# Performance work log

Hardware: AMD Instinct MI355X
Metric: run time of the kernel (lower is better)

Reference implementation:

```python
import jax, jax.numpy as jnp
import numpy as np

DIM = 1024
NUM_HEADS = 16
HEAD_DIM = DIM // NUM_HEADS  # 64
SCALE = float(np.sqrt(HEAD_DIM))


def setup_inputs() -> dict:
    key = jax.random.key(0)
    k1, k2, k3, k4 = jax.random.split(key, 4)
    B, N = 2, 2048
    x = jax.random.normal(k1, (B, N, DIM), dtype=jnp.float32)
    # torch nn.Linear weights are [out_features, in_features]
    w_qkv = jax.random.normal(k2, (3 * DIM, DIM), dtype=jnp.float32) * (1.0 / np.sqrt(DIM))
    w_proj = jax.random.normal(k3, (DIM, DIM), dtype=jnp.float32) * (1.0 / np.sqrt(DIM))
    b_proj = jax.random.normal(k4, (DIM,), dtype=jnp.float32) * 0.02
    return {"x": x, "w_qkv": w_qkv, "w_proj": w_proj, "b_proj": b_proj}


def reference(x, w_qkv, w_proj, b_proj):
    B, N, C = x.shape
    H, D = NUM_HEADS, HEAD_DIM
    # qkv linear (no bias): [B,N,3C]
    qkv = jnp.einsum('bnc,oc->bno', x, w_qkv)
    qkv = qkv.reshape(B, N, 3, H, D).transpose(2, 0, 3, 1, 4)  # [3,B,H,N,D]
    q, k, v = qkv[0], qkv[1], qkv[2]
    attn = jnp.einsum('bhnd,bhmd->bhnm', q, k) / SCALE  # [B,H,N,N]
    attn = jax.nn.softmax(attn, axis=-1)
    out = jnp.einsum('bhnm,bhmd->bhnd', attn, v)  # [B,H,N,D]
    out = out.transpose(0, 2, 1, 3).reshape(B, N, C)
    return jnp.einsum('bnc,oc->bno', out, w_proj) + b_proj
```

## Files before the change

### kernel.cpp

```cpp
#include <hip/hip_runtime.h>


typedef __bf16 bf16x8 __attribute__((ext_vector_type(8)));
typedef __bf16 bf16x4 __attribute__((ext_vector_type(4)));
typedef float f32x4 __attribute__((ext_vector_type(4)));

#define NTOK 2048
#define MFMA16(a, b, c) __builtin_amdgcn_mfma_f32_16x16x32_bf16((a), (b), (c), 0, 0, 0)

#define WAITBAR(N)                                         \
    asm volatile("s_waitcnt vmcnt(" #N ")" ::: "memory"); \
    __builtin_amdgcn_s_barrier();                          \
    __builtin_amdgcn_sched_barrier(0)

__device__ __forceinline__ unsigned short f2bf(float f) {
    unsigned int u = __float_as_uint(f);
    u = (u + 0x7FFFu + ((u >> 16) & 1u)) >> 16;
    return (unsigned short)u;
}

__device__ __forceinline__ float hw_exp2(float x) {
#if __has_builtin(__builtin_amdgcn_exp2f)
    return __builtin_amdgcn_exp2f(x);
#else
    float r;
    asm("v_exp_f32 %0, %1" : "=v"(r) : "v"(x));
    return r;
#endif
}

__device__ __forceinline__ void gload16(const void* g, void* l) {
    __builtin_amdgcn_global_load_lds(
        (__attribute__((address_space(1))) void*)(g),
        (__attribute__((address_space(3))) void*)(l), 16, 0, 0);
}

__global__ __launch_bounds__(256) void cast3_kernel(
    const float* __restrict__ x, const float* __restrict__ wq,
    const float* __restrict__ wp, unsigned short* __restrict__ xb,
    unsigned short* __restrict__ wqb, unsigned short* __restrict__ wpb) {
    const int NX = 1048576, NWQ = 786432;
    int i = blockIdx.x * 256 + threadIdx.x;
    const float* src;
    unsigned short* dst;
    int j;
    if (i < NX) { src = x; dst = xb; j = i; }
    else if (i < NX + NWQ) { src = wq; dst = wqb; j = i - NX; }
    else { src = wp; dst = wpb; j = i - NX - NWQ; }
    const float4 v = reinterpret_cast<const float4*>(src)[j];
    ushort4 o;
    o.x = f2bf(v.x); o.y = f2bf(v.y); o.z = f2bf(v.z); o.w = f2bf(v.w);
    reinterpret_cast<ushort4*>(dst)[j] = o;
}

template <int EPI>
__global__ __launch_bounds__(512) void gemm_bt_kernel(
    const unsigned short* __restrict__ A, const unsigned short* __restrict__ B,
    int K, int Ncols,
    unsigned short* __restrict__ q_out, unsigned short* __restrict__ k_out,
    unsigned short* __restrict__ vt_out,
    float* __restrict__ c_out, const float* __restrict__ bias) {
    __shared__ __align__(16) char smem[49152];
    const int tid = threadIdx.x;
    const int l = tid & 63;
    const int wid = tid >> 6;
    const int c = l & 15, g = l >> 4;
    const int wr = wid >> 2, wc = wid & 3;
    const int m0 = blockIdx.x * 128, n0 = blockIdx.y * 128;

    f32x4 acc[4][2] = {};

    const int srow = tid >> 2;
    const int sc16 = (tid & 3) ^ (srow & 3);
    auto STAGE = [&](int bi, int kt) {
        gload16(A + (size_t)(m0 + srow) * K + kt + sc16 * 8,
                smem + bi * 8192 + wid * 1024);
        gload16(B + (size_t)(n0 + srow) * K + kt + sc16 * 8,
                smem + 24576 + bi * 8192 + wid * 1024);
    };

    auto COMPUTE = [&](int bi) {
        const char* bA = smem + bi * 8192;
        const char* bB = smem + 24576 + bi * 8192;
        bf16x8 af[4], bfr[2];
#pragma unroll
        for (int m = 0; m < 4; ++m) {
            const int row = wr * 64 + m * 16 + c;
            af[m] = *(const bf16x8*)(bA + row * 64 + (g ^ (row & 3)) * 16);
        }
#pragma unroll
        for (int n = 0; n < 2; ++n) {
            const int row = wc * 32 + n * 16 + c;
            bfr[n] = *(const bf16x8*)(bB + row * 64 + (g ^ (row & 3)) * 16);
        }
#pragma unroll
        for (int m = 0; m < 4; ++m)
#pragma unroll
            for (int n = 0; n < 2; ++n)
                acc[m][n] = MFMA16(af[m], bfr[n], acc[m][n]);
    };

    const int NK = K >> 5;
    STAGE(0, 0);
    STAGE(1, 32);
    int cb = 0, sb = 2;
    for (int it = 0; it < NK - 2; ++it) {
        WAITBAR(2);
        STAGE(sb, (it + 2) * 32);
        COMPUTE(cb);
        cb = cb == 2 ? 0 : cb + 1;
        sb = sb == 2 ? 0 : sb + 1;
    }
    WAITBAR(2);
    COMPUTE(cb);
    cb = cb == 2 ? 0 : cb + 1;
    WAITBAR(0);
    COMPUTE(cb);

    if (EPI == 0 && n0 >= 2048) {
        __syncthreads();
#pragma unroll
        for (int m = 0; m < 4; ++m) {
            const int tl0 = wr * 64 + m * 16 + g * 4;
#pragma unroll
            for (int n = 0; n < 2; ++n) {
                const int oc = wc * 32 + n * 16 + c;
                bf16x4 pv;
#pragma unroll
                for (int r = 0; r < 4; ++r) pv[r] = (__bf16)acc[m][n][r];
                *(bf16x4*)(smem + oc * 256 + ((tl0 * 2) ^ ((oc & 7) << 4))) = pv;
            }
        }
        __syncthreads();
        const int b = m0 >> 11;
        const int mloc = m0 & 2047;
#pragma unroll
        for (int qq = 0; qq < 4; ++qq) {
            const int ci = qq * 512 + tid;
            const int oc = ci >> 4, j16 = ci & 15;
            const int o = n0 + oc;
            const int head = b * 16 + ((o >> 6) & 15), d = o & 63;
            const bf16x4* src = (const bf16x4*)(smem + oc * 256 +
                                                ((j16 * 16) ^ ((oc & 7) << 4)));
            const int tl8 = j16 * 8;
            const int tpb = (tl8 & ~63) | (tl8 & 0x20) | ((tl8 & 0x10) >> 2) |
                            ((tl8 & 0x08) << 1);
            unsigned short* orow = vt_out + ((size_t)head * 64 + d) * NTOK + mloc;
            *(bf16x4*)(orow + tpb) = src[0];
            *(bf16x4*)(orow + tpb + 8) = src[1];
        }
        return;
    }

#pragma unroll
    for (int m = 0; m < 4; ++m) {
        const int gmb = m0 + wr * 64 + m * 16 + (g << 2);
#pragma unroll
        for (int n = 0; n < 2; ++n) {
            const int gn = n0 + wc * 32 + n * 16 + c;
            if (EPI == 0) {
                const int which = gn >> 10;
                const int h = (gn >> 6) & 15, d = gn & 63;
#pragma unroll
                for (int r = 0; r < 4; ++r) {
                    const int gm = gmb + r;
                    const int head = ((gm >> 11) << 4) | h;
                    const int t = gm & 2047;
                    const float v = acc[m][n][r];
                    if (which == 0)
                        q_out[((size_t)head * NTOK + t) * 64 + d] =
                            f2bf(v * 0.18033688011f);
                    else
                        k_out[((size_t)head * NTOK + t) * 64 + d] = f2bf(v);
                }
            } else {
                const float bv = bias[gn];
#pragma unroll
                for (int r = 0; r < 4; ++r)
                    c_out[(size_t)(gmb + r) * Ncols + gn] = acc[m][n][r] + bv;
            }
        }
    }
}

__global__ __launch_bounds__(256) void attn_kernel(
    const unsigned short* __restrict__ Qb, const unsigned short* __restrict__ Kb,
    const unsigned short* __restrict__ Vt, unsigned short* __restrict__ Ob) {
    __shared__ __align__(16) unsigned short ldsK[3][64 * 64];
    __shared__ __align__(16) unsigned short ldsV[3][64 * 64];

    const int tid = threadIdx.x, l = tid & 63, wid = tid >> 6;
    const int c = l & 15, g = l >> 4;
    const int head = blockIdx.x;
    const int q0 = blockIdx.y * 128 + wid * 32;

    const unsigned short* Qh = Qb + (size_t)head * NTOK * 64;
    const unsigned short* Kh = Kb + (size_t)head * NTOK * 64;
    const unsigned short* Vh = Vt + (size_t)head * 64 * NTOK;

    bf16x8 qf[2][2];
#pragma unroll
    for (int mq = 0; mq < 2; ++mq)
#pragma unroll
        for (int kk = 0; kk < 2; ++kk)
            qf[mq][kk] = *(const bf16x8*)(Qh + (size_t)(q0 + mq * 16 + c) * 64 +
                                          kk * 32 + g * 8);

    f32x4 o_acc[2][4] = {};
    f32x4 lsum[2] = {};

    const int srow = tid >> 3;

    auto STAGE = [&](int bi, int kbase) {
#pragma unroll
        for (int r = 0; r < 2; ++r) {
            const int row = r * 32 + srow;
            const int slot = (tid & 7) ^ (row & 7);
            gload16(Kh + (size_t)(kbase + row) * 64 + slot * 8,
                    (char*)ldsK + bi * 8192 + wid * 1024 + r * 4096);
            gload16(Vh + (size_t)row * NTOK + kbase + slot * 8,
                    (char*)ldsV + bi * 8192 + wid * 1024 + r * 4096);
        }
    };

    auto COMPUTE = [&](int bi) {
        const char* baseK = (const char*)ldsK + bi * 8192;
        const char* baseV = (const char*)ldsV + bi * 8192;
        f32x4 s0[4] = {}, s1[4] = {};
#pragma unroll
        for (int mk = 0; mk < 4; ++mk) {
            const int row = mk * 16 + c;
#pragma unroll
            for (int kk = 0; kk < 2; ++kk) {
                const int slot = (kk * 4 + g) ^ (row & 7);
                const bf16x8 kf = *(const bf16x8*)(baseK + row * 128 + slot * 16);
                s0[mk] = MFMA16(kf, qf[0][kk], s0[mk]);
                s1[mk] = MFMA16(kf, qf[1][kk], s1[mk]);
            }
        }
        bf16x8 pkw0[2], pkw1[2];
#pragma unroll
        for (int mk = 0; mk < 4; ++mk) {
            const int kv = mk >> 1, hh = (mk & 1) * 4;
            {
                const float p0 = hw_exp2(s0[mk][0]);
                const float p1 = hw_exp2(s0[mk][1]);
                const float p2 = hw_exp2(s0[mk][2]);
                const float p3 = hw_exp2(s0[mk][3]);
                lsum[0][0] += p0; lsum[0][1] += p1; lsum[0][2] += p2; lsum[0][3] += p3;
                pkw0[kv][hh + 0] = (__bf16)p0; pkw0[kv][hh + 1] = (__bf16)p1;
                pkw0[kv][hh + 2] = (__bf16)p2; pkw0[kv][hh + 3] = (__bf16)p3;
            }
            {
                const float p0 = hw_exp2(s1[mk][0]);
                const float p1 = hw_exp2(s1[mk][1]);
                const float p2 = hw_exp2(s1[mk][2]);
                const float p3 = hw_exp2(s1[mk][3]);
                lsum[1][0] += p0; lsum[1][1] += p1; lsum[1][2] += p2; lsum[1][3] += p3;
                pkw1[kv][hh + 0] = (__bf16)p0; pkw1[kv][hh + 1] = (__bf16)p1;
                pkw1[kv][hh + 2] = (__bf16)p2; pkw1[kv][hh + 3] = (__bf16)p3;
            }
        }
#pragma unroll
        for (int dm = 0; dm < 4; ++dm) {
            const int row = dm * 16 + c;
#pragma unroll
            for (int kv = 0; kv < 2; ++kv) {
                const int slot = (kv * 4 + g) ^ (row & 7);
                const bf16x8 vt = *(const bf16x8*)(baseV + row * 128 + slot * 16);
                o_acc[0][dm] = MFMA16(vt, pkw0[kv], o_acc[0][dm]);
                o_acc[1][dm] = MFMA16(vt, pkw1[kv], o_acc[1][dm]);
            }
        }
    };

    STAGE(0, 0);
    STAGE(1, 64);
    int cb = 0, sb = 2;
    for (int it = 0; it < 30; ++it) {
        WAITBAR(4);
        STAGE(sb, (it + 2) * 64);
        COMPUTE(cb);
        cb = cb == 2 ? 0 : cb + 1;
        sb = sb == 2 ? 0 : sb + 1;
    }
    WAITBAR(4);
    COMPUTE(0);
    WAITBAR(0);
    COMPUTE(1);

    const int b = head >> 4, h = head & 15;
#pragma unroll
    for (int mq = 0; mq < 2; ++mq) {
        float lr = (lsum[mq][0] + lsum[mq][1]) + (lsum[mq][2] + lsum[mq][3]);
        lr += __shfl_xor(lr, 16);
        lr += __shfl_xor(lr, 32);
        const float inv = 1.f / lr;
        unsigned short* orow =
            Ob + ((size_t)b * NTOK + q0 + mq * 16 + c) * 1024 + h * 64;
#pragma unroll
        for (int dm = 0; dm < 4; ++dm) {
            bf16x4 ov;
#pragma unroll
            for (int r = 0; r < 4; ++r) ov[r] = (__bf16)(o_acc[mq][dm][r] * inv);
            *(bf16x4*)(orow + dm * 16 + g * 4) = ov;
        }
    }
}

extern "C" void kernel_launch(void* const* d_in, const int* in_sizes, int n_in,
                              void* d_out, int out_size, void* d_ws, size_t ws_size,
                              hipStream_t stream) {
    const float* x = (const float*)d_in[0];
    const float* w_qkv = (const float*)d_in[1];
    const float* w_proj = (const float*)d_in[2];
    const float* b_proj = (const float*)d_in[3];
    float* out = (float*)d_out;

    char* ws = (char*)d_ws;
    const size_t MB = 1 << 20;
    unsigned short* xb = (unsigned short*)(ws);
    unsigned short* wqkvb = (unsigned short*)(ws + 8 * MB);
    unsigned short* wpb = (unsigned short*)(ws + 14 * MB);
    unsigned short* Qb = (unsigned short*)(ws + 16 * MB);
    unsigned short* Kb = (unsigned short*)(ws + 24 * MB);
    unsigned short* Vt = (unsigned short*)(ws + 32 * MB);
    unsigned short* attnb = xb;

    cast3_kernel<<<8192, 256, 0, stream>>>(x, w_qkv, w_proj, xb, wqkvb, wpb);

    gemm_bt_kernel<0><<<dim3(32, 24), 512, 0, stream>>>(
        xb, wqkvb, 1024, 3072, Qb, Kb, Vt, nullptr, nullptr);

    attn_kernel<<<dim3(32, 16), 256, 0, stream>>>(Qb, Kb, Vt, attnb);

    gemm_bt_kernel<1><<<dim3(32, 8), 512, 0, stream>>>(
        attnb, wpb, 1024, 1024, nullptr, nullptr, nullptr, out, b_proj);
}
```

Baseline: 108.6 us.

## Switch attention K/V staging to double buffering and pack bf16 conversions

The attention loop drops the three-deep K/V LDS ring, with its explicit vmcnt-counted waits, in favor of a simple two-buffer ping-pong. Each iteration prefetches the next tile and ends with a __syncthreads, and LDS use falls from 48KB to 32KB. The exp'd probabilities are now converted to bf16 in pairs with v_cvt_pk_bf16_f32 instead of per-element casts, to cut VALU conversion work. The cost is a shallower prefetch: only one tile is in flight, and each iteration waits for the full load before the barrier, which may expose memory latency.

```diff
diff --git a/kernel.cpp b/kernel.cpp
--- a/kernel.cpp
+++ b/kernel.cpp
@@ -4,6 +4,8 @@
 typedef __bf16 bf16x8 __attribute__((ext_vector_type(8)));
 typedef __bf16 bf16x4 __attribute__((ext_vector_type(4)));
 typedef float f32x4 __attribute__((ext_vector_type(4)));
+typedef unsigned int u32;
+typedef u32 u32x4 __attribute__((ext_vector_type(4)));
 
 #define NTOK 2048
 #define MFMA16(a, b, c) __builtin_amdgcn_mfma_f32_16x16x32_bf16((a), (b), (c), 0, 0, 0)
@@ -17,6 +19,12 @@
     unsigned int u = __float_as_uint(f);
     u = (u + 0x7FFFu + ((u >> 16) & 1u)) >> 16;
     return (unsigned short)u;
+}
+
+__device__ __forceinline__ u32 cvt_pk(float lo, float hi) {
+    u32 r;
+    asm("v_cvt_pk_bf16_f32 %0, %1, %2" : "=v"(r) : "v"(lo), "v"(hi));
+    return r;
 }
 
 __device__ __forceinline__ float hw_exp2(float x) {
@@ -186,8 +194,8 @@
 __global__ __launch_bounds__(256) void attn_kernel(
     const unsigned short* __restrict__ Qb, const unsigned short* __restrict__ Kb,
     const unsigned short* __restrict__ Vt, unsigned short* __restrict__ Ob) {
-    __shared__ __align__(16) unsigned short ldsK[3][64 * 64];
-    __shared__ __align__(16) unsigned short ldsV[3][64 * 64];
+    __shared__ __align__(16) unsigned short ldsK[2][64 * 64];
+    __shared__ __align__(16) unsigned short ldsV[2][64 * 64];
 
     const int tid = threadIdx.x, l = tid & 63, wid = tid >> 6;
     const int c = l & 15, g = l >> 4;
@@ -211,21 +219,25 @@
 
     const int srow = tid >> 3;
 
-    auto STAGE = [&](int bi, int kbase) {
+    auto STAGE = [&](int buf, int kbase) {
 #pragma unroll
         for (int r = 0; r < 2; ++r) {
             const int row = r * 32 + srow;
             const int slot = (tid & 7) ^ (row & 7);
             gload16(Kh + (size_t)(kbase + row) * 64 + slot * 8,
-                    (char*)ldsK + bi * 8192 + wid * 1024 + r * 4096);
+                    (char*)ldsK[buf] + wid * 1024 + r * 4096);
             gload16(Vh + (size_t)row * NTOK + kbase + slot * 8,
-                    (char*)ldsV + bi * 8192 + wid * 1024 + r * 4096);
+                    (char*)ldsV[buf] + wid * 1024 + r * 4096);
         }
     };
 
-    auto COMPUTE = [&](int bi) {
-        const char* baseK = (const char*)ldsK + bi * 8192;
-        const char* baseV = (const char*)ldsV + bi * 8192;
+    STAGE(0, 0);
+    __syncthreads();
+
+    int cur = 0;
+    for (int it = 0; it < 32; ++it) {
+        if (it + 1 < 32) STAGE(cur ^ 1, (it + 1) * 64);
+
         f32x4 s0[4] = {}, s1[4] = {};
 #pragma unroll
         for (int mk = 0; mk < 4; ++mk) {
@@ -233,61 +245,52 @@
 #pragma unroll
             for (int kk = 0; kk < 2; ++kk) {
                 const int slot = (kk * 4 + g) ^ (row & 7);
-                const bf16x8 kf = *(const bf16x8*)(baseK + row * 128 + slot * 16);
+                const bf16x8 kf =
+                    *(const bf16x8*)((const char*)ldsK[cur] + row * 128 + slot * 16);
                 s0[mk] = MFMA16(kf, qf[0][kk], s0[mk]);
                 s1[mk] = MFMA16(kf, qf[1][kk], s1[mk]);
             }
         }
-        bf16x8 pkw0[2], pkw1[2];
+
+        u32x4 pw0[2], pw1[2];
 #pragma unroll
         for (int mk = 0; mk < 4; ++mk) {
-            const int kv = mk >> 1, hh = (mk & 1) * 4;
+            const int kv = mk >> 1, dw = (mk & 1) * 2;
             {
-                const float p0 = hw_exp2(s0[mk][0]);
-                const float p1 = hw_exp2(s0[mk][1]);
-                const float p2 = hw_exp2(s0[mk][2]);
-                const float p3 = hw_exp2(s0[mk][3]);
-                lsum[0][0] += p0; lsum[0][1] += p1; lsum[0][2] += p2; lsum[0][3] += p3;
-                pkw0[kv][hh + 0] = (__bf16)p0; pkw0[kv][hh + 1] = (__bf16)p1;
-                pkw0[kv][hh + 2] = (__bf16)p2; pkw0[kv][hh + 3] = (__bf16)p3;
+                f32x4 e;
+                e[0] = hw_exp2(s0[mk][0]); e[1] = hw_exp2(s0[mk][1]);
+                e[2] = hw_exp2(s0[mk][2]); e[3] = hw_exp2(s0[mk][3]);
+                lsum[0] += e;
+                pw0[kv][dw + 0] = cvt_pk(e[0], e[1]);
+                pw0[kv][dw + 1] = cvt_pk(e[2], e[3]);
             }
             {
-                const float p0 = hw_exp2(s1[mk][0]);
-                const float p1 = hw_exp2(s1[mk][1]);
-                const float p2 = hw_exp2(s1[mk][2]);
-                const float p3 = hw_exp2(s1[mk][3]);
-                lsum[1][0] += p0; lsum[1][1] += p1; lsum[1][2] += p2; lsum[1][3] += p3;
-                pkw1[kv][hh + 0] = (__bf16)p0; pkw1[kv][hh + 1] = (__bf16)p1;
-                pkw1[kv][hh + 2] = (__bf16)p2; pkw1[kv][hh + 3] = (__bf16)p3;
-            }
-        }
+                f32x4 e;
+                e[0] = hw_exp2(s1[mk][0]); e[1] = hw_exp2(s1[mk][1]);
+                e[2] = hw_exp2(s1[mk][2]); e[3] = hw_exp2(s1[mk][3]);
+                lsum[1] += e;
+                pw1[kv][dw + 0] = cvt_pk(e[0], e[1]);
+                pw1[kv][dw + 1] = cvt_pk(e[2], e[3]);
+            }
+        }
+
 #pragma unroll
         for (int dm = 0; dm < 4; ++dm) {
             const int row = dm * 16 + c;
 #pragma unroll
             for (int kv = 0; kv < 2; ++kv) {
                 const int slot = (kv * 4 + g) ^ (row & 7);
-                const bf16x8 vt = *(const bf16x8*)(baseV + row * 128 + slot * 16);
-                o_acc[0][dm] = MFMA16(vt, pkw0[kv], o_acc[0][dm]);
-                o_acc[1][dm] = MFMA16(vt, pkw1[kv], o_acc[1][dm]);
-            }
-        }
-    };
-
-    STAGE(0, 0);
-    STAGE(1, 64);
-    int cb = 0, sb = 2;
-    for (int it = 0; it < 30; ++it) {
-        WAITBAR(4);
-        STAGE(sb, (it + 2) * 64);
-        COMPUTE(cb);
-        cb = cb == 2 ? 0 : cb + 1;
-        sb = sb == 2 ? 0 : sb + 1;
-    }
-    WAITBAR(4);
-    COMPUTE(0);
-    WAITBAR(0);
-    COMPUTE(1);
+                const bf16x8 vt =
+                    *(const bf16x8*)((const char*)ldsV[cur] + row * 128 + slot * 16);
+                o_acc[0][dm] = MFMA16(vt, __builtin_bit_cast(bf16x8, pw0[kv]),
+                                      o_acc[0][dm]);
+                o_acc[1][dm] = MFMA16(vt, __builtin_bit_cast(bf16x8, pw1[kv]),
+                                      o_acc[1][dm]);
+            }
+        }
+        __syncthreads();
+        cur ^= 1;
+    }
 
     const int b = head >> 4, h = head & 15;
 #pragma unroll
```

Result: no change. 108.1 us (-0.4%).
